# Kernel tuning notes

Measured on AMD Instinct MI355X. Metric: run time of the kernel, lower is better.

## Reference

```python
import jax, jax.numpy as jnp
import numpy as np

N, M, NBR = 20000, 12, 64
AF, ORIG, H, B, K = 256, 92, 256, 200, 50
N_CONV = 3
EPS = 1e-5


def _bn_train(x, gamma, beta):
    mu = x.mean(0)
    var = x.var(0)  # biased, matches torch BN normalization in train mode
    return (x - mu) * jax.lax.rsqrt(var + EPS) * gamma + beta


def _conv_layer(atom_in, nbr_fea, nbr_idx, w1, b1, w2, b2, gamma, beta):
    n, m = nbr_idx.shape
    m1 = m // 2
    atom_nbr = atom_in[nbr_idx]                     # [N, M, AF]
    atom_u = jnp.broadcast_to(atom_in[:, None, :], (n, m1, atom_in.shape[-1]))
    an1, an2 = atom_nbr[:, :m1], atom_nbr[:, m1:]
    nf1, nf2 = nbr_fea[:, :m1], nbr_fea[:, m1:]
    u1 = jnp.concatenate([atom_u, an1, nf1], axis=2)  # [N, M1, 2*AF+NBR]
    u2 = jnp.concatenate([atom_u, an2, nf2], axis=2)
    g1 = jax.nn.relu(jnp.einsum('nmf,fo->nmo', u1, w1) + b1)
    g2 = jax.nn.softplus(jnp.einsum('nmf,fo->nmo', u2, w1) + b1)
    nbr_sumed = g1.sum(1) + g2.sum(1)               # sum over all M neighbors, [N, 2*AF]
    nbr_sumed = nbr_sumed @ w2 + b2                 # [N, AF]
    nbr_sumed = _bn_train(nbr_sumed, gamma, beta)
    return jax.nn.softplus(atom_in + nbr_sumed)


def setup_inputs() -> dict:
    key = jax.random.key(0)
    ks = jax.random.split(key, 16)
    inp = {
        'atom_fea': jax.random.normal(ks[0], (N, ORIG), jnp.float32),
        'nbr_fea': jax.random.normal(ks[1], (N, M, NBR), jnp.float32),
        'nbr_fea_idx': jax.random.randint(ks[2], (N, M), 0, N),
        'M1_index': jax.random.randint(ks[3], (B * K,), 0, N),
        'seg_ids': jnp.repeat(jnp.arange(B), K),
        'm2_fea': jax.random.normal(ks[4], (B, 4), jnp.float32),
        'emb_w': jax.random.normal(ks[5], (ORIG, AF), jnp.float32) * 0.05,
        'emb_b': jnp.zeros((AF,), jnp.float32),
        'w1': jax.random.normal(ks[6], (N_CONV, 2 * AF + NBR, 2 * AF), jnp.float32) * 0.05,
        'b1': jnp.zeros((N_CONV, 2 * AF), jnp.float32),
        'w2': jax.random.normal(ks[7], (N_CONV, 2 * AF, AF), jnp.float32) * 0.05,
        'b2': jnp.zeros((N_CONV, AF), jnp.float32),
        'gamma': jnp.ones((N_CONV, AF), jnp.float32),
        'beta': jnp.zeros((N_CONV, AF), jnp.float32),
        'fc_w': jax.random.normal(ks[8], (AF + 4, H), jnp.float32) * 0.05,
        'fc_b': jnp.zeros((H,), jnp.float32),
        'out_w': jax.random.normal(ks[9], (H, 1), jnp.float32) * 0.05,
        'out_b': jnp.zeros((1,), jnp.float32),
    }
    return inp


def reference(atom_fea, nbr_fea, nbr_fea_idx, M1_index, seg_ids, m2_fea,
              emb_w, emb_b, w1, b1, w2, b2, gamma, beta,
              fc_w, fc_b, out_w, out_b):
    x = jax.nn.softplus(atom_fea @ emb_w + emb_b)           # [N, AF]
    for i in range(N_CONV):
        x = _conv_layer(x, nbr_fea, nbr_fea_idx, w1[i], b1[i], w2[i], b2[i], gamma[i], beta[i])
    m1_fea = x[M1_index]                                    # [B*K, AF]
    sums = jax.ops.segment_sum(m1_fea, seg_ids, num_segments=B)
    counts = jax.ops.segment_sum(jnp.ones((m1_fea.shape[0], 1), m1_fea.dtype), seg_ids, num_segments=B)
    crys = sums / counts                                    # per-crystal mean, [B, AF]
    crys = jnp.concatenate([crys, m2_fea], axis=1)          # [B, AF+4]
    h = jax.nn.softplus(jax.nn.softplus(crys) @ fc_w + fc_b)
    out = h @ out_w + out_b                                 # [B, 1]
    return out
```

## Files before the change

kernel.cpp:

```cpp
#include <hip/hip_runtime.h>
#include <hip/hip_bf16.h>


#define N_ATOM 20000
#define AF     256
#define F2     512
#define ORIG   92
#define ORIG_P 96
#define BB     200
#define KK     50
#define BN_EPS 1e-5f
#define ZS     132

#define OFF_B1   0
#define OFF_B2   1536
#define OFF_GAM  2304
#define OFF_BET  3072
#define OFF_EMBB 3840
#define OFF_FCB  4096
#define OFF_FCW  4352
#define OFF_OW   70912
#define OFF_OB   71168
#define OFF_M2   71169
#define N_SMALL  71969

using bf16x8 = __attribute__((ext_vector_type(8))) short;
using f32x4  = __attribute__((ext_vector_type(4))) float;

__device__ __forceinline__ float bf2f(__hip_bfloat16 v) { return __bfloat162float(v); }
__device__ __forceinline__ __hip_bfloat16 f2bf(float v) { return __float2bfloat16(v); }
__device__ __forceinline__ unsigned short f2bfbits(float f) {
    unsigned u = __float_as_uint(f);
    u += 0x7fffu + ((u >> 16) & 1u);
    return (unsigned short)(u >> 16);
}
__device__ __forceinline__ float bfbits2f(unsigned short u) {
    return __uint_as_float(((unsigned)u) << 16);
}
__device__ __forceinline__ float softplus_f(float x) {
    return fmaxf(x, 0.f) + __logf(1.f + __expf(-fabsf(x)));
}
__device__ __forceinline__ float ld_any(const void* p, long idx, bool isf32) {
    return isf32 ? ((const float*)p)[idx] : bf2f(((const __hip_bfloat16*)p)[idx]);
}

__global__ void detect_dtype(const unsigned* __restrict__ gamma_raw,
                             unsigned* __restrict__ flag) {
    unsigned u = gamma_raw[0];
    flag[0] = ((u & 0xFFFFu) == 0u) ? 1u : 0u;
}

__global__ __launch_bounds__(256) void prep_nf(const void* __restrict__ nf,
                                               const unsigned* __restrict__ dflag,
                                               unsigned* __restrict__ out) {
    bool isf32 = dflag[0] != 0u;
    int idx = blockIdx.x * 256 + threadIdx.x;
    if (idx >= N_ATOM * 12 * 64 / 4) return;
    if (isf32) {
        float4 v = ((const float4*)nf)[idx];
        out[idx * 2]     = (unsigned)f2bfbits(v.x) | ((unsigned)f2bfbits(v.y) << 16);
        out[idx * 2 + 1] = (unsigned)f2bfbits(v.z) | ((unsigned)f2bfbits(v.w) << 16);
    } else {
        uint2 v = ((const uint2*)nf)[idx];
        ((uint2*)out)[idx] = v;
    }
}

__global__ __launch_bounds__(256) void prep_pad_af(const void* __restrict__ af,
                                                   const unsigned* __restrict__ dflag,
                                                   __hip_bfloat16* __restrict__ out) {
    bool isf32 = dflag[0] != 0u;
    int i = blockIdx.x * 256 + threadIdx.x;
    if (i >= N_ATOM * ORIG_P) return;
    int r = i / ORIG_P, k = i - r * ORIG_P;
    out[i] = (k < ORIG) ? f2bf(ld_any(af, (long)r * ORIG + k, isf32)) : f2bf(0.f);
}
__global__ __launch_bounds__(256) void prep_t_emb(const void* __restrict__ w,
                                                  const unsigned* __restrict__ dflag,
                                                  __hip_bfloat16* __restrict__ out) {
    bool isf32 = dflag[0] != 0u;
    int i = blockIdx.x * 256 + threadIdx.x;
    if (i >= AF * ORIG_P) return;
    int n = i / ORIG_P, k = i - n * ORIG_P;
    out[i] = (k < ORIG) ? f2bf(ld_any(w, (long)k * AF + n, isf32)) : f2bf(0.f);
}
__global__ __launch_bounds__(256) void prep_t_w1(const void* __restrict__ w,
                                                 const unsigned* __restrict__ dflag,
                                                 __hip_bfloat16* __restrict__ out) {
    bool isf32 = dflag[0] != 0u;
    int i = blockIdx.x * 256 + threadIdx.x;
    if (i >= 3 * F2 * 576) return;
    int l = i / (F2 * 576); int rem = i - l * (F2 * 576);
    int c = rem / 576, k = rem - c * 576;
    out[i] = f2bf(ld_any(w, (long)l * 576 * F2 + (long)k * F2 + c, isf32));
}
__global__ __launch_bounds__(256) void prep_t_w2(const void* __restrict__ w,
                                                 const unsigned* __restrict__ dflag,
                                                 __hip_bfloat16* __restrict__ out) {
    bool isf32 = dflag[0] != 0u;
    int i = blockIdx.x * 256 + threadIdx.x;
    if (i >= 3 * AF * F2) return;
    int l = i / (AF * F2); int rem = i - l * (AF * F2);
    int n = rem / F2, k = rem - n * F2;
    out[i] = f2bf(ld_any(w, (long)l * F2 * AF + (long)k * AF + n, isf32));
}
__global__ __launch_bounds__(256)
void prep_smalls(const void* b1, const void* b2, const void* gam, const void* bet,
                 const void* embb, const void* fcb, const void* fcw,
                 const void* ow, const void* ob, const void* m2,
                 const unsigned* __restrict__ dflag,
                 __hip_bfloat16* __restrict__ s) {
    bool isf32 = dflag[0] != 0u;
    int i = blockIdx.x * 256 + threadIdx.x;
    if (i >= N_SMALL) return;
    float v;
    if      (i < OFF_B2)   v = ld_any(b1,   i - OFF_B1,  isf32);
    else if (i < OFF_GAM)  v = ld_any(b2,   i - OFF_B2,  isf32);
    else if (i < OFF_BET)  v = ld_any(gam,  i - OFF_GAM, isf32);
    else if (i < OFF_EMBB) v = ld_any(bet,  i - OFF_BET, isf32);
    else if (i < OFF_FCB)  v = ld_any(embb, i - OFF_EMBB,isf32);
    else if (i < OFF_OW)   v = (i < OFF_FCW) ? ld_any(fcb, i - OFF_FCB, isf32)
                                             : ld_any(fcw, i - OFF_FCW, isf32);
    else if (i < OFF_OB)   v = ld_any(ow,   i - OFF_OW,  isf32);
    else if (i < OFF_M2)   v = ld_any(ob,   i - OFF_OB,  isf32);
    else                   v = ld_any(m2,   i - OFF_M2,  isf32);
    s[i] = f2bf(v);
}

template <bool OUT_BF16>
__global__ __launch_bounds__(256)
void gemm_kernel(const __hip_bfloat16* __restrict__ A, int lda,
                 const __hip_bfloat16* __restrict__ BT, int ldb,
                 void* __restrict__ Cp, int M, int N, int K,
                 const __hip_bfloat16* __restrict__ bias, int act,
                 float* __restrict__ st) {
    __shared__ __align__(16) unsigned short sA[128 * 40];
    __shared__ __align__(16) unsigned short sB[128 * 40];
    __shared__ float sS[128], sS2[128];
    int tid  = threadIdx.x;
    int mt   = blockIdx.x, nt = blockIdx.y;
    int wave = tid >> 6, lane = tid & 63, q = lane >> 4, ln = lane & 15;
    int wr   = wave >> 1, wc = wave & 1;

    if (st && tid < 128) { sS[tid] = 0.f; sS2[tid] = 0.f; }

    f32x4 acc[4][4];
    for (int i = 0; i < 4; i++)
        for (int j = 0; j < 4; j++) acc[i][j] = (f32x4){0.f, 0.f, 0.f, 0.f};

    for (int k0 = 0; k0 < K; k0 += 32) {
        for (int i = tid; i < 512; i += 256) {
            int r = i >> 2, ch = i & 3;
            int row = mt * 128 + r;
            uint4 va = make_uint4(0u, 0u, 0u, 0u);
            if (row < M) va = *(const uint4*)(A + (size_t)row * lda + k0 + ch * 8);
            *(uint4*)(&sA[r * 40 + ch * 8]) = va;
            int n = nt * 128 + r;
            uint4 vb = *(const uint4*)(BT + (size_t)n * ldb + k0 + ch * 8);
            *(uint4*)(&sB[r * 40 + ch * 8]) = vb;
        }
        __syncthreads();
        bf16x8 af[4], bf[4];
        for (int i = 0; i < 4; i++)
            af[i] = *(const bf16x8*)(&sA[(wr * 64 + i * 16 + ln) * 40 + q * 8]);
        for (int j = 0; j < 4; j++)
            bf[j] = *(const bf16x8*)(&sB[(wc * 64 + j * 16 + ln) * 40 + q * 8]);
        for (int i = 0; i < 4; i++)
            for (int j = 0; j < 4; j++)
                acc[i][j] = __builtin_amdgcn_mfma_f32_16x16x32_bf16(af[i], bf[j], acc[i][j], 0, 0, 0);
        __syncthreads();
    }
    for (int j = 0; j < 4; j++) {
        int cl  = wc * 64 + j * 16 + ln;
        int col = nt * 128 + cl;
        float bv = bias ? bf2f(bias[col]) : 0.f;
        float ls = 0.f, ls2 = 0.f;
        for (int i = 0; i < 4; i++) {
            for (int r = 0; r < 4; r++) {
                int row = mt * 128 + wr * 64 + i * 16 + q * 4 + r;
                if (row >= M) continue;
                float v = acc[i][j][r] + bv;
                if (st) { ls += v; ls2 += v * v; }
                if (act == 1) v = softplus_f(v);
                if (OUT_BF16) ((__hip_bfloat16*)Cp)[(size_t)row * N + col] = f2bf(v);
                else          ((float*)Cp)[(size_t)row * N + col] = v;
            }
        }
        if (st) { atomicAdd(&sS[cl], ls); atomicAdd(&sS2[cl], ls2); }
    }
    if (st) {
        __syncthreads();
        if (tid < 128) {
            int col = nt * 128 + tid;
            atomicAdd(&st[col], sS[tid]);
            atomicAdd(&st[AF + col], sS2[tid]);
        }
    }
}

__global__ __launch_bounds__(256)
void conv_fused(const void* __restrict__ nf,
                const unsigned* __restrict__ dflag,
                int prepped,
                const int* __restrict__ nidx,
                const __hip_bfloat16* __restrict__ xa,
                const __hip_bfloat16* __restrict__ y,
                const __hip_bfloat16* __restrict__ w1Tl,
                __hip_bfloat16* __restrict__ ns)
{
    __shared__ __align__(16) unsigned short smem[96 * 72 + 128 * 72];
    unsigned short* sNF = smem;
    unsigned short* sBT = smem + 96 * 72;
    unsigned short* sZ  = smem;
    __shared__ int sIdx[96];

    int tid = threadIdx.x;
    int ab  = blockIdx.x * 8;
    int cb  = blockIdx.y * 128;

    if (prepped || dflag[0] == 0u) {
        const __hip_bfloat16* nfB = (const __hip_bfloat16*)nf;
        for (int i = tid; i < 96 * 8; i += 256) {
            int r = i >> 3, ch = i & 7;
            uint4 v = *(const uint4*)(nfB + (size_t)(ab * 12 + r) * 64 + ch * 8);
            *(uint4*)(&sNF[r * 72 + ch * 8]) = v;
        }
    } else {
        const float* nfF = (const float*)nf;
        for (int i = tid; i < 96 * 8; i += 256) {
            int r = i >> 3, ch = i & 7;
            const float* src = nfF + (size_t)(ab * 12 + r) * 64 + ch * 8;
            float4 v0 = *(const float4*)(src);
            float4 v1 = *(const float4*)(src + 4);
            unsigned short* d = &sNF[r * 72 + ch * 8];
            d[0] = f2bfbits(v0.x); d[1] = f2bfbits(v0.y);
            d[2] = f2bfbits(v0.z); d[3] = f2bfbits(v0.w);
            d[4] = f2bfbits(v1.x); d[5] = f2bfbits(v1.y);
            d[6] = f2bfbits(v1.z); d[7] = f2bfbits(v1.w);
        }
    }
    for (int i = tid; i < 128 * 8; i += 256) {
        int c = i >> 3, ch = i & 7;
        uint4 v = *(const uint4*)(w1Tl + (size_t)(cb + c) * 576 + 512 + ch * 8);
        *(uint4*)(&sBT[c * 72 + ch * 8]) = v;
    }
    if (tid < 96) sIdx[tid] = nidx[ab * 12 + tid];
    __syncthreads();

    int wave = tid >> 6, lane = tid & 63, q = lane >> 4, ln = lane & 15;
    int c0 = wave * 32;

    bf16x8 bfr[2][2];
    for (int ct = 0; ct < 2; ct++)
        for (int ks = 0; ks < 2; ks++)
            bfr[ct][ks] = *(const bf16x8*)(&sBT[(c0 + ct * 16 + ln) * 72 + ks * 32 + q * 8]);

    f32x4 acc[6][2];
    for (int rt = 0; rt < 6; rt++)
        for (int ct = 0; ct < 2; ct++) acc[rt][ct] = (f32x4){0.f, 0.f, 0.f, 0.f};
    for (int rt = 0; rt < 6; rt++) {
        bf16x8 a0 = *(const bf16x8*)(&sNF[(rt * 16 + ln) * 72 + q * 8]);
        bf16x8 a1 = *(const bf16x8*)(&sNF[(rt * 16 + ln) * 72 + 32 + q * 8]);
        acc[rt][0] = __builtin_amdgcn_mfma_f32_16x16x32_bf16(a0, bfr[0][0], acc[rt][0], 0, 0, 0);
        acc[rt][0] = __builtin_amdgcn_mfma_f32_16x16x32_bf16(a1, bfr[0][1], acc[rt][0], 0, 0, 0);
        acc[rt][1] = __builtin_amdgcn_mfma_f32_16x16x32_bf16(a0, bfr[1][0], acc[rt][1], 0, 0, 0);
        acc[rt][1] = __builtin_amdgcn_mfma_f32_16x16x32_bf16(a1, bfr[1][1], acc[rt][1], 0, 0, 0);
    }
    __syncthreads();

    for (int rt = 0; rt < 6; rt++)
        for (int ct = 0; ct < 2; ct++)
            for (int r = 0; r < 4; r++)
                sZ[(rt * 16 + q * 4 + r) * ZS + c0 + ct * 16 + ln] = f2bfbits(acc[rt][ct][r]);
    __syncthreads();

    int a  = tid >> 5, ch = tid & 31;
    int n  = ab + a;
    int gc = cb + ch * 4;
    uint2 xau = *(const uint2*)(xa + (size_t)n * F2 + gc);
    float xa0 = bfbits2f((unsigned short)(xau.x & 0xffff));
    float xa1 = bfbits2f((unsigned short)(xau.x >> 16));
    float xa2 = bfbits2f((unsigned short)(xau.y & 0xffff));
    float xa3 = bfbits2f((unsigned short)(xau.y >> 16));
    float r0 = 0.f, r1 = 0.f, r2 = 0.f, r3 = 0.f;
#pragma unroll
    for (int m = 0; m < 12; m++) {
        int gi = sIdx[a * 12 + m];
        uint2 zz = *(const uint2*)(&sZ[(a * 12 + m) * ZS + ch * 4]);
        uint2 yy = *(const uint2*)(y + (size_t)gi * F2 + gc);
        float v0 = bfbits2f((unsigned short)(zz.x & 0xffff)) + xa0 +
                   bfbits2f((unsigned short)(yy.x & 0xffff));
        float v1 = bfbits2f((unsigned short)(zz.x >> 16)) + xa1 +
                   bfbits2f((unsigned short)(yy.x >> 16));
        float v2 = bfbits2f((unsigned short)(zz.y & 0xffff)) + xa2 +
                   bfbits2f((unsigned short)(yy.y & 0xffff));
        float v3 = bfbits2f((unsigned short)(zz.y >> 16)) + xa3 +
                   bfbits2f((unsigned short)(yy.y >> 16));
        if (m < 6) {
            v0 = fmaxf(v0, 0.f); v1 = fmaxf(v1, 0.f);
            v2 = fmaxf(v2, 0.f); v3 = fmaxf(v3, 0.f);
        } else {
            v0 = softplus_f(v0); v1 = softplus_f(v1);
            v2 = softplus_f(v2); v3 = softplus_f(v3);
        }
        r0 += v0; r1 += v1; r2 += v2; r3 += v3;
    }
    uint2 o;
    o.x = (unsigned)f2bfbits(r0) | ((unsigned)f2bfbits(r1) << 16);
    o.y = (unsigned)f2bfbits(r2) | ((unsigned)f2bfbits(r3) << 16);
    *(uint2*)(ns + (size_t)n * F2 + gc) = o;
}

__global__ __launch_bounds__(256)
void bn_apply(const float* __restrict__ h2, const float* __restrict__ st,
              const __hip_bfloat16* __restrict__ x,
              const __hip_bfloat16* __restrict__ gamma,
              const __hip_bfloat16* __restrict__ beta,
              __hip_bfloat16* __restrict__ xo) {
    int i = blockIdx.x * 256 + threadIdx.x;
    int c = i & 255;
    float mu  = st[c] * (1.f / 20000.f);
    float var = fmaxf(st[AF + c] * (1.f / 20000.f) - mu * mu, 0.f);
    float t = (h2[i] - mu) * rsqrtf(var + BN_EPS) * bf2f(gamma[c]) + bf2f(beta[c]);
    xo[i] = f2bf(softplus_f(bf2f(x[i]) + t));
}

__global__ __launch_bounds__(256)
void readout(const __hip_bfloat16* __restrict__ x, const int* __restrict__ m1,
             const __hip_bfloat16* __restrict__ smalls,
             const unsigned* __restrict__ dflag,
             void* __restrict__ outp) {
    __shared__ float sc[AF + 4];
    __shared__ float sred[4];
    bool isf32 = dflag[0] != 0u;
    int b = blockIdx.x, tid = threadIdx.x;
    float s = 0.f;
    for (int j = 0; j < KK; j++) {
        int row = m1[b * KK + j];
        s += bf2f(x[(size_t)row * AF + tid]);
    }
    sc[tid] = softplus_f(s * (1.f / (float)KK));
    if (tid < 4) sc[AF + tid] = softplus_f(bf2f(smalls[OFF_M2 + b * 4 + tid]));
    __syncthreads();
    float acc = bf2f(smalls[OFF_FCB + tid]);
    for (int k = 0; k < AF + 4; k++) acc += sc[k] * bf2f(smalls[OFF_FCW + k * 256 + tid]);
    float h = softplus_f(acc);
    float v = h * bf2f(smalls[OFF_OW + tid]);
    for (int off = 32; off > 0; off >>= 1) v += __shfl_down(v, off);
    if ((tid & 63) == 0) sred[tid >> 6] = v;
    __syncthreads();
    if (tid == 0) {
        float o = sred[0] + sred[1] + sred[2] + sred[3] + bf2f(smalls[OFF_OB]);
        if (isf32) ((float*)outp)[b] = o;
        else       ((__hip_bfloat16*)outp)[b] = f2bf(o);
    }
}

extern "C" void kernel_launch(void* const* d_in, const int* in_sizes, int n_in,
                              void* d_out, int out_size, void* d_ws, size_t ws_size,
                              hipStream_t stream) {
    const void* atom_fea = d_in[0];
    const void* nbr_fea  = d_in[1];
    const int*  nbr_idx  = (const int*)d_in[2];
    const int*  m1_idx   = (const int*)d_in[3];
    const void* m2_fea = d_in[5];
    const void* emb_w  = d_in[6];
    const void* emb_b  = d_in[7];
    const void* w1     = d_in[8];
    const void* b1     = d_in[9];
    const void* w2     = d_in[10];
    const void* b2     = d_in[11];
    const void* gamma  = d_in[12];
    const void* beta   = d_in[13];
    const void* fc_w   = d_in[14];
    const void* fc_b   = d_in[15];
    const void* out_w  = d_in[16];
    const void* out_b  = d_in[17];

    char* ws = (char*)d_ws;
    size_t off = 0;
    auto alloc = [&](size_t bytes) -> char* {
        char* p = ws + off;
        off += (bytes + 255) & ~(size_t)255;
        return p;
    };
    __hip_bfloat16* w1T    = (__hip_bfloat16*)alloc((size_t)3 * F2 * 576 * 2);
    __hip_bfloat16* w2T    = (__hip_bfloat16*)alloc((size_t)3 * AF * F2 * 2);
    __hip_bfloat16* smalls = (__hip_bfloat16*)alloc((size_t)N_SMALL * 2);
    __hip_bfloat16* xb0    = (__hip_bfloat16*)alloc((size_t)N_ATOM * AF * 2);
    __hip_bfloat16* xb1    = (__hip_bfloat16*)alloc((size_t)N_ATOM * AF * 2);
    char*           regX   = alloc((size_t)N_ATOM * F2 * 2);
    char*           regY   = alloc((size_t)N_ATOM * F2 * 2);
    char*           regZ   = alloc((size_t)N_ATOM * F2 * 2);
    float*          stats  = (float*)alloc((size_t)3 * 2 * AF * 4);
    unsigned*       dflag  = (unsigned*)alloc(256);
    size_t core_end = off;
    char*           nfb    = alloc((size_t)N_ATOM * 12 * 64 * 2);
    int use_nfb = (ws_size >= off) ? 1 : 0;

    __hip_bfloat16* xa     = (__hip_bfloat16*)regX;
    float*          h2     = (float*)regX;
    __hip_bfloat16* af_pad = (__hip_bfloat16*)regY;
    __hip_bfloat16* yb     = (__hip_bfloat16*)regY;
    __hip_bfloat16* embT   = (__hip_bfloat16*)regZ;
    __hip_bfloat16* nsb    = (__hip_bfloat16*)regZ;
    (void)core_end;

    detect_dtype<<<1, 1, 0, stream>>>((const unsigned*)gamma, dflag);
    (void)hipMemsetAsync(stats, 0, (size_t)3 * 2 * AF * 4, stream);

    if (use_nfb)
        prep_nf<<<(N_ATOM * 12 * 64 / 4 + 255) / 256, 256, 0, stream>>>(nbr_fea, dflag,
                                                                        (unsigned*)nfb);
    prep_pad_af<<<(N_ATOM * ORIG_P + 255) / 256, 256, 0, stream>>>(atom_fea, dflag, af_pad);
    prep_t_emb<<<(AF * ORIG_P + 255) / 256, 256, 0, stream>>>(emb_w, dflag, embT);
    prep_t_w1<<<(3 * F2 * 576 + 255) / 256, 256, 0, stream>>>(w1, dflag, w1T);
    prep_t_w2<<<(3 * AF * F2 + 255) / 256, 256, 0, stream>>>(w2, dflag, w2T);
    prep_smalls<<<(N_SMALL + 255) / 256, 256, 0, stream>>>(b1, b2, gamma, beta, emb_b,
                                                           fc_b, fc_w, out_w, out_b, m2_fea,
                                                           dflag, smalls);

    dim3 g_emb((N_ATOM + 127) / 128, AF / 128);
    gemm_kernel<true><<<g_emb, 256, 0, stream>>>(af_pad, ORIG_P, embT, ORIG_P,
                                                 xb0, N_ATOM, AF, ORIG_P,
                                                 smalls + OFF_EMBB, 1, nullptr);

    const void* nf_conv = use_nfb ? (const void*)nfb : nbr_fea;

    __hip_bfloat16* xc = xb0;
    __hip_bfloat16* xn = xb1;
    for (int l = 0; l < 3; l++) {
        const __hip_bfloat16* w1Tl = w1T + (size_t)l * F2 * 576;
        dim3 gxy((N_ATOM + 127) / 128, F2 / 128);
        gemm_kernel<true><<<gxy, 256, 0, stream>>>(xc, AF, w1Tl, 576,
                                                   xa, N_ATOM, F2, AF,
                                                   smalls + OFF_B1 + l * F2, 0, nullptr);
        gemm_kernel<true><<<gxy, 256, 0, stream>>>(xc, AF, w1Tl + 256, 576,
                                                   yb, N_ATOM, F2, AF, nullptr, 0, nullptr);
        dim3 gconv(N_ATOM / 8, F2 / 128);
        conv_fused<<<gconv, 256, 0, stream>>>(nf_conv, dflag, use_nfb, nbr_idx,
                                              xa, yb, w1Tl, nsb);
        float* stl = stats + l * 2 * AF;
        dim3 gh2((N_ATOM + 127) / 128, AF / 128);
        gemm_kernel<false><<<gh2, 256, 0, stream>>>(nsb, F2, w2T + (size_t)l * AF * F2, F2,
                                                    h2, N_ATOM, AF, F2,
                                                    smalls + OFF_B2 + l * AF, 0, stl);
        bn_apply<<<(N_ATOM * AF) / 256, 256, 0, stream>>>(h2, stl, xc,
                                                          smalls + OFF_GAM + l * AF,
                                                          smalls + OFF_BET + l * AF, xn);
        __hip_bfloat16* t = xc; xc = xn; xn = t;
    }
    readout<<<BB, 256, 0, stream>>>(xc, m1_idx, smalls, dflag, d_out);
}
```

Baseline: 677.8 us.

## Loop column tiles inside conv_fused and store pre-BN activations as bf16

conv_fused now handles all four 128-column tiles of the 512-wide gated output in a single block. It loads the neighbor-feature tile and indices once instead of once per column block, which cuts the grid to one dimension. The second GEMM now writes h2 in bf16 rather than fp32, and bn_apply processes four elements per thread with vector loads, roughly halving its memory traffic. In exchange, each conv block runs serially over more work with more barriers, and the BN inputs lose precision from bf16 rounding before normalization, while the statistics still come from the GEMM epilogue.

```diff
diff --git a/kernel.cpp b/kernel.cpp
--- a/kernel.cpp
+++ b/kernel.cpp
@@ -208,15 +208,14 @@
                 const __hip_bfloat16* __restrict__ w1Tl,
                 __hip_bfloat16* __restrict__ ns)
 {
-    __shared__ __align__(16) unsigned short smem[96 * 72 + 128 * 72];
-    unsigned short* sNF = smem;
-    unsigned short* sBT = smem + 96 * 72;
-    unsigned short* sZ  = smem;
+    __shared__ __align__(16) unsigned short sNF[96 * 72];
+    __shared__ __align__(16) unsigned short sR[96 * ZS];
     __shared__ int sIdx[96];
+    unsigned short* sBT = sR;
+    unsigned short* sZ  = sR;
 
     int tid = threadIdx.x;
     int ab  = blockIdx.x * 8;
-    int cb  = blockIdx.y * 128;
 
     if (prepped || dflag[0] == 0u) {
         const __hip_bfloat16* nfB = (const __hip_bfloat16*)nf;
@@ -239,90 +238,110 @@
             d[6] = f2bfbits(v1.z); d[7] = f2bfbits(v1.w);
         }
     }
-    for (int i = tid; i < 128 * 8; i += 256) {
-        int c = i >> 3, ch = i & 7;
-        uint4 v = *(const uint4*)(w1Tl + (size_t)(cb + c) * 576 + 512 + ch * 8);
-        *(uint4*)(&sBT[c * 72 + ch * 8]) = v;
-    }
     if (tid < 96) sIdx[tid] = nidx[ab * 12 + tid];
-    __syncthreads();
 
     int wave = tid >> 6, lane = tid & 63, q = lane >> 4, ln = lane & 15;
     int c0 = wave * 32;
-
-    bf16x8 bfr[2][2];
-    for (int ct = 0; ct < 2; ct++)
-        for (int ks = 0; ks < 2; ks++)
-            bfr[ct][ks] = *(const bf16x8*)(&sBT[(c0 + ct * 16 + ln) * 72 + ks * 32 + q * 8]);
-
-    f32x4 acc[6][2];
-    for (int rt = 0; rt < 6; rt++)
-        for (int ct = 0; ct < 2; ct++) acc[rt][ct] = (f32x4){0.f, 0.f, 0.f, 0.f};
-    for (int rt = 0; rt < 6; rt++) {
-        bf16x8 a0 = *(const bf16x8*)(&sNF[(rt * 16 + ln) * 72 + q * 8]);
-        bf16x8 a1 = *(const bf16x8*)(&sNF[(rt * 16 + ln) * 72 + 32 + q * 8]);
-        acc[rt][0] = __builtin_amdgcn_mfma_f32_16x16x32_bf16(a0, bfr[0][0], acc[rt][0], 0, 0, 0);
-        acc[rt][0] = __builtin_amdgcn_mfma_f32_16x16x32_bf16(a1, bfr[0][1], acc[rt][0], 0, 0, 0);
-        acc[rt][1] = __builtin_amdgcn_mfma_f32_16x16x32_bf16(a0, bfr[1][0], acc[rt][1], 0, 0, 0);
-        acc[rt][1] = __builtin_amdgcn_mfma_f32_16x16x32_bf16(a1, bfr[1][1], acc[rt][1], 0, 0, 0);
-    }
-    __syncthreads();
-
-    for (int rt = 0; rt < 6; rt++)
-        for (int ct = 0; ct < 2; ct++)
-            for (int r = 0; r < 4; r++)
-                sZ[(rt * 16 + q * 4 + r) * ZS + c0 + ct * 16 + ln] = f2bfbits(acc[rt][ct][r]);
-    __syncthreads();
-
-    int a  = tid >> 5, ch = tid & 31;
+    int a  = tid >> 5, chc = tid & 31;
     int n  = ab + a;
-    int gc = cb + ch * 4;
-    uint2 xau = *(const uint2*)(xa + (size_t)n * F2 + gc);
-    float xa0 = bfbits2f((unsigned short)(xau.x & 0xffff));
-    float xa1 = bfbits2f((unsigned short)(xau.x >> 16));
-    float xa2 = bfbits2f((unsigned short)(xau.y & 0xffff));
-    float xa3 = bfbits2f((unsigned short)(xau.y >> 16));
-    float r0 = 0.f, r1 = 0.f, r2 = 0.f, r3 = 0.f;
+
+    for (int ct = 0; ct < 4; ct++) {
+        int cb = ct * 128;
+        __syncthreads();
+        for (int i = tid; i < 128 * 8; i += 256) {
+            int c = i >> 3, ch = i & 7;
+            uint4 v = *(const uint4*)(w1Tl + (size_t)(cb + c) * 576 + 512 + ch * 8);
+            *(uint4*)(&sBT[c * 72 + ch * 8]) = v;
+        }
+        __syncthreads();
+
+        bf16x8 bfr[2][2];
+        for (int c2 = 0; c2 < 2; c2++)
+            for (int ks = 0; ks < 2; ks++)
+                bfr[c2][ks] = *(const bf16x8*)(&sBT[(c0 + c2 * 16 + ln) * 72 + ks * 32 + q * 8]);
+
+        f32x4 acc[6][2];
+        for (int rt = 0; rt < 6; rt++)
+            for (int c2 = 0; c2 < 2; c2++) acc[rt][c2] = (f32x4){0.f, 0.f, 0.f, 0.f};
+        for (int rt = 0; rt < 6; rt++) {
+            bf16x8 a0 = *(const bf16x8*)(&sNF[(rt * 16 + ln) * 72 + q * 8]);
+            bf16x8 a1 = *(const bf16x8*)(&sNF[(rt * 16 + ln) * 72 + 32 + q * 8]);
+            acc[rt][0] = __builtin_amdgcn_mfma_f32_16x16x32_bf16(a0, bfr[0][0], acc[rt][0], 0, 0, 0);
+            acc[rt][0] = __builtin_amdgcn_mfma_f32_16x16x32_bf16(a1, bfr[0][1], acc[rt][0], 0, 0, 0);
+            acc[rt][1] = __builtin_amdgcn_mfma_f32_16x16x32_bf16(a0, bfr[1][0], acc[rt][1], 0, 0, 0);
+            acc[rt][1] = __builtin_amdgcn_mfma_f32_16x16x32_bf16(a1, bfr[1][1], acc[rt][1], 0, 0, 0);
+        }
+        __syncthreads();
+
+        for (int rt = 0; rt < 6; rt++)
+            for (int c2 = 0; c2 < 2; c2++)
+                for (int r = 0; r < 4; r++)
+                    sZ[(rt * 16 + q * 4 + r) * ZS + c0 + c2 * 16 + ln] = f2bfbits(acc[rt][c2][r]);
+        __syncthreads();
+
+        int gc = cb + chc * 4;
+        uint2 xau = *(const uint2*)(xa + (size_t)n * F2 + gc);
+        float xa0 = bfbits2f((unsigned short)(xau.x & 0xffff));
+        float xa1 = bfbits2f((unsigned short)(xau.x >> 16));
+        float xa2 = bfbits2f((unsigned short)(xau.y & 0xffff));
+        float xa3 = bfbits2f((unsigned short)(xau.y >> 16));
+        float r0 = 0.f, r1 = 0.f, r2 = 0.f, r3 = 0.f;
 #pragma unroll
-    for (int m = 0; m < 12; m++) {
-        int gi = sIdx[a * 12 + m];
-        uint2 zz = *(const uint2*)(&sZ[(a * 12 + m) * ZS + ch * 4]);
-        uint2 yy = *(const uint2*)(y + (size_t)gi * F2 + gc);
-        float v0 = bfbits2f((unsigned short)(zz.x & 0xffff)) + xa0 +
-                   bfbits2f((unsigned short)(yy.x & 0xffff));
-        float v1 = bfbits2f((unsigned short)(zz.x >> 16)) + xa1 +
-                   bfbits2f((unsigned short)(yy.x >> 16));
-        float v2 = bfbits2f((unsigned short)(zz.y & 0xffff)) + xa2 +
-                   bfbits2f((unsigned short)(yy.y & 0xffff));
-        float v3 = bfbits2f((unsigned short)(zz.y >> 16)) + xa3 +
-                   bfbits2f((unsigned short)(yy.y >> 16));
-        if (m < 6) {
-            v0 = fmaxf(v0, 0.f); v1 = fmaxf(v1, 0.f);
-            v2 = fmaxf(v2, 0.f); v3 = fmaxf(v3, 0.f);
-        } else {
-            v0 = softplus_f(v0); v1 = softplus_f(v1);
-            v2 = softplus_f(v2); v3 = softplus_f(v3);
-        }
-        r0 += v0; r1 += v1; r2 += v2; r3 += v3;
-    }
-    uint2 o;
-    o.x = (unsigned)f2bfbits(r0) | ((unsigned)f2bfbits(r1) << 16);
-    o.y = (unsigned)f2bfbits(r2) | ((unsigned)f2bfbits(r3) << 16);
-    *(uint2*)(ns + (size_t)n * F2 + gc) = o;
+        for (int m = 0; m < 12; m++) {
+            int gi = sIdx[a * 12 + m];
+            uint2 zz = *(const uint2*)(&sZ[(a * 12 + m) * ZS + chc * 4]);
+            uint2 yy = *(const uint2*)(y + (size_t)gi * F2 + gc);
+            float v0 = bfbits2f((unsigned short)(zz.x & 0xffff)) + xa0 +
+                       bfbits2f((unsigned short)(yy.x & 0xffff));
+            float v1 = bfbits2f((unsigned short)(zz.x >> 16)) + xa1 +
+                       bfbits2f((unsigned short)(yy.x >> 16));
+            float v2 = bfbits2f((unsigned short)(zz.y & 0xffff)) + xa2 +
+                       bfbits2f((unsigned short)(yy.y & 0xffff));
+            float v3 = bfbits2f((unsigned short)(zz.y >> 16)) + xa3 +
+                       bfbits2f((unsigned short)(yy.y >> 16));
+            if (m < 6) {
+                v0 = fmaxf(v0, 0.f); v1 = fmaxf(v1, 0.f);
+                v2 = fmaxf(v2, 0.f); v3 = fmaxf(v3, 0.f);
+            } else {
+                v0 = softplus_f(v0); v1 = softplus_f(v1);
+                v2 = softplus_f(v2); v3 = softplus_f(v3);
+            }
+            r0 += v0; r1 += v1; r2 += v2; r3 += v3;
+        }
+        uint2 o;
+        o.x = (unsigned)f2bfbits(r0) | ((unsigned)f2bfbits(r1) << 16);
+        o.y = (unsigned)f2bfbits(r2) | ((unsigned)f2bfbits(r3) << 16);
+        *(uint2*)(ns + (size_t)n * F2 + gc) = o;
+    }
 }
 
 __global__ __launch_bounds__(256)
-void bn_apply(const float* __restrict__ h2, const float* __restrict__ st,
+void bn_apply(const __hip_bfloat16* __restrict__ h2, const float* __restrict__ st,
               const __hip_bfloat16* __restrict__ x,
               const __hip_bfloat16* __restrict__ gamma,
               const __hip_bfloat16* __restrict__ beta,
               __hip_bfloat16* __restrict__ xo) {
-    int i = blockIdx.x * 256 + threadIdx.x;
+    int i = (blockIdx.x * 256 + threadIdx.x) * 4;
     int c = i & 255;
-    float mu  = st[c] * (1.f / 20000.f);
-    float var = fmaxf(st[AF + c] * (1.f / 20000.f) - mu * mu, 0.f);
-    float t = (h2[i] - mu) * rsqrtf(var + BN_EPS) * bf2f(gamma[c]) + bf2f(beta[c]);
-    xo[i] = f2bf(softplus_f(bf2f(x[i]) + t));
+    uint2 hv = *(const uint2*)(h2 + i);
+    uint2 xv = *(const uint2*)(x + i);
+    uint2 o;
+    float r[4];
+#pragma unroll
+    for (int k = 0; k < 4; k++) {
+        int cc = c + k;
+        float mu  = st[cc] * (1.f / 20000.f);
+        float var = fmaxf(st[AF + cc] * (1.f / 20000.f) - mu * mu, 0.f);
+        unsigned hh = (k < 2) ? hv.x : hv.y;
+        unsigned xx = (k < 2) ? xv.x : xv.y;
+        float h = bfbits2f((unsigned short)((k & 1) ? (hh >> 16) : (hh & 0xffff)));
+        float xf = bfbits2f((unsigned short)((k & 1) ? (xx >> 16) : (xx & 0xffff)));
+        float t = (h - mu) * rsqrtf(var + BN_EPS) * bf2f(gamma[cc]) + bf2f(beta[cc]);
+        r[k] = softplus_f(xf + t);
+    }
+    o.x = (unsigned)f2bfbits(r[0]) | ((unsigned)f2bfbits(r[1]) << 16);
+    o.y = (unsigned)f2bfbits(r[2]) | ((unsigned)f2bfbits(r[3]) << 16);
+    *(uint2*)(xo + i) = o;
 }
 
 __global__ __launch_bounds__(256)
@@ -394,17 +413,15 @@
     char*           regZ   = alloc((size_t)N_ATOM * F2 * 2);
     float*          stats  = (float*)alloc((size_t)3 * 2 * AF * 4);
     unsigned*       dflag  = (unsigned*)alloc(256);
-    size_t core_end = off;
     char*           nfb    = alloc((size_t)N_ATOM * 12 * 64 * 2);
     int use_nfb = (ws_size >= off) ? 1 : 0;
 
     __hip_bfloat16* xa     = (__hip_bfloat16*)regX;
-    float*          h2     = (float*)regX;
+    __hip_bfloat16* h2     = (__hip_bfloat16*)regX;
     __hip_bfloat16* af_pad = (__hip_bfloat16*)regY;
     __hip_bfloat16* yb     = (__hip_bfloat16*)regY;
     __hip_bfloat16* embT   = (__hip_bfloat16*)regZ;
     __hip_bfloat16* nsb    = (__hip_bfloat16*)regZ;
-    (void)core_end;
 
     detect_dtype<<<1, 1, 0, stream>>>((const unsigned*)gamma, dflag);
     (void)hipMemsetAsync(stats, 0, (size_t)3 * 2 * AF * 4, stream);
@@ -437,17 +454,16 @@
                                                    smalls + OFF_B1 + l * F2, 0, nullptr);
         gemm_kernel<true><<<gxy, 256, 0, stream>>>(xc, AF, w1Tl + 256, 576,
                                                    yb, N_ATOM, F2, AF, nullptr, 0, nullptr);
-        dim3 gconv(N_ATOM / 8, F2 / 128);
-        conv_fused<<<gconv, 256, 0, stream>>>(nf_conv, dflag, use_nfb, nbr_idx,
-                                              xa, yb, w1Tl, nsb);
+        conv_fused<<<N_ATOM / 8, 256, 0, stream>>>(nf_conv, dflag, use_nfb, nbr_idx,
+                                                   xa, yb, w1Tl, nsb);
         float* stl = stats + l * 2 * AF;
         dim3 gh2((N_ATOM + 127) / 128, AF / 128);
-        gemm_kernel<false><<<gh2, 256, 0, stream>>>(nsb, F2, w2T + (size_t)l * AF * F2, F2,
-                                                    h2, N_ATOM, AF, F2,
-                                                    smalls + OFF_B2 + l * AF, 0, stl);
-        bn_apply<<<(N_ATOM * AF) / 256, 256, 0, stream>>>(h2, stl, xc,
-                                                          smalls + OFF_GAM + l * AF,
-                                                          smalls + OFF_BET + l * AF, xn);
+        gemm_kernel<true><<<gh2, 256, 0, stream>>>(nsb, F2, w2T + (size_t)l * AF * F2, F2,
+                                                   h2, N_ATOM, AF, F2,
+                                                   smalls + OFF_B2 + l * AF, 0, stl);
+        bn_apply<<<(N_ATOM * AF / 4) / 256, 256, 0, stream>>>(h2, stl, xc,
+                                                              smalls + OFF_GAM + l * AF,
+                                                              smalls + OFF_BET + l * AF, xn);
         __hip_bfloat16* t = xc; xc = xn; xn = t;
     }
     readout<<<BB, 256, 0, stream>>>(xc, m1_idx, smalls, dflag, d_out);
```

New measurement: 646.4 us. 4.6% less time.
